# Performance work log

Hardware: AMD Instinct MI355X
Metric: run time of the kernel (lower is better)

The kernel has to match this reference:

```python
import jax, jax.numpy as jnp
from jax import lax
import numpy as np

N_BASIS = 256
N_FREQ = 128
N_TIME = 8
LAM = 0.2
LR = 1e-3
B1, B2, EPS = 0.9, 0.999, 1e-8
CONV_TOL = 1e-3


def setup_inputs() -> dict:
    key = jax.random.key(0)
    k1, k2 = jax.random.split(key)
    spec = jax.random.normal(k1, (32, N_FREQ, 256), dtype=jnp.float32)
    basis = jax.random.normal(k2, (N_FREQ * N_TIME, N_BASIS), dtype=jnp.float32)
    return {"spec": spec, "basis": basis, "n_iter_coef": 30, "pad": 0, "stride": 4}


def normalize01(x):
    # torch normalize01 with dims=-1, keepdims
    xmin = x.min(axis=-1, keepdims=True)
    xmax = x.max(axis=-1, keepdims=True)
    return (x - xmin) / (xmax - xmin)


def _response(x, basis, n_iter):
    # x: [B, D]; Adam-optimize coef [B, N_BASIS] for n_iter steps with the
    # same early-stop rule as the torch code (frozen via a done flag).
    B = x.shape[0]
    sig = jnp.std(x, ddof=1)  # torch .std() is unbiased over all elements

    def loss_fn(coef):
        pred = coef @ basis.T                      # [B, D]
        mse = jnp.mean((pred - x) ** 2)
        return mse + LAM * sig * jnp.mean(jnp.abs(coef / sig))

    coef0 = jnp.full((B, N_BASIS), 0.5 / N_BASIS, dtype=jnp.float32)
    m0 = jnp.zeros_like(coef0)
    v0 = jnp.zeros_like(coef0)

    def body(carry, _):
        coef, m, v, t, old_loss, done = carry
        loss, g = jax.value_and_grad(loss_fn)(coef)
        t_new = t + 1.0
        m_new = B1 * m + (1.0 - B1) * g
        v_new = B2 * v + (1.0 - B2) * g * g
        mhat = m_new / (1.0 - B1 ** t_new)
        vhat = v_new / (1.0 - B2 ** t_new)
        coef_new = coef - LR * mhat / (jnp.sqrt(vhat) + EPS)
        conv = jnp.abs(old_loss - loss) / old_loss < CONV_TOL
        sel = lambda a, b: jnp.where(done, a, b)
        new_carry = (
            sel(coef, coef_new),
            sel(m, m_new),
            sel(v, v_new),
            jnp.where(done, t, t_new),
            jnp.where(done, old_loss, loss),
            done | conv,
        )
        return new_carry, None

    init = (coef0, m0, v0, jnp.float32(0.0), jnp.float32(1e-10), jnp.array(False))
    (coef, _, _, _, _, _), _ = lax.scan(body, init, None, length=n_iter)
    return coef  # detached in torch


def reference(spec, basis, n_iter_coef, pad, stride):
    if spec.ndim == 2:
        spec = spec[None, ...]
    B, F, T = spec.shape
    spec_ = jnp.pad(spec, ((0, 0), (0, 0), (pad, pad)))
    starts = np.arange(0, T - N_TIME + 1, stride)          # window start frames
    idx = starts[:, None] + np.arange(N_TIME)              # [W, N_TIME]
    wins = spec_[:, :, idx]                                # [B, F, W, N_TIME]
    x = jnp.transpose(wins, (2, 0, 1, 3)).reshape(len(starts), B, F * N_TIME)
    x = normalize01(x)                                     # per row of [B, D]
    coef = jax.vmap(lambda xw: _response(xw, basis, n_iter_coef))(x)  # [W, B, N_BASIS]
    return jnp.transpose(coef, (1, 2, 0))                  # [B, N_BASIS, W]
```

## Files before the change

kernel.cpp:

```cpp
#include <hip/hip_runtime.h>
#include <math.h>

#define NB     256
#define NF     128
#define FT     1024
#define NW     63
#define TORIG  256
#define MAXIT  48
#define RPB    8
#define NBLK   4
#define GRID   256

__device__ __forceinline__ float rl(float v, int lane) {
    return __uint_as_float((unsigned)__builtin_amdgcn_readlane((int)__float_as_uint(v), lane));
}

__device__ __forceinline__ int xidx(int k2, int cg, int row) {
    return (k2 * 512 + row * 64 + (cg ^ row)) * 4;
}

__global__ __launch_bounds__(512, 2) void window_kernel(
    const float* __restrict__ spec,
    const float* __restrict__ basis,
    float* __restrict__ G,
    const int* __restrict__ p_niter,
    const int* __restrict__ p_pad,
    const int* __restrict__ p_stride,
    double* __restrict__ sxbuf,
    double* __restrict__ gpart,
    unsigned int* __restrict__ gcnt,
    float* __restrict__ out)
{
    __shared__ float  s_p0[RPB * 2048];
    __shared__ float  s_p1[RPB * 2048];
    __shared__ float  s_gred[2][NB];
    __shared__ float  s_mn[RPB], s_rng[RPB];
    __shared__ double s_dred[8];
    __shared__ float  s_redq[2][8], s_redr[2][8];
    __shared__ unsigned int s_wcnt[2];
    __shared__ int    s_stop[2];
    float* const s_xn = s_p1;

    const int bid = blockIdx.x;
    const int yy  = bid >> 3;
    const int q   = yy & 3;
    const int w   = (bid & 7) + 8 * (yy >> 2);
    const int tid = threadIdx.x;
    const int ks  = tid >> 6;
    const int kg  = tid & 63;
    const int r   = kg >> 3;
    const int cgo = 8 * ks + (kg & 7);
    const int n_iter = p_niter[0];
    const int t0     = w * p_stride[0] - p_pad[0];
    unsigned int* gbar = gcnt + MAXIT * NW;

    {
        const int c = tid & 255, jh = tid >> 8;
        float acc = 0.f;
        const float* bp = basis + (size_t)(jh * 512) * NB;
        #pragma unroll 16
        for (int j = 0; j < 512; ++j)
            acc = fmaf(bp[j * NB + bid], bp[j * NB + c], acc);
        s_gred[jh][c] = acc;
        __syncthreads();
        if (jh == 0) G[(size_t)bid * NB + c] = s_gred[0][c] + s_gred[1][c];
    }
    __threadfence();
    __syncthreads();
    if (tid == 0) atomicAdd(gbar, 1u);
    if (w >= NW) return;

    #pragma unroll
    for (int i = 0; i < 16; ++i) {
        const int e = i * 512 + tid;
        const int b = e >> 10, jj = e & 1023;
        const int f = jj >> 3, t = jj & 7, tq = t0 + t;
        s_xn[b * FT + jj] = (tq >= 0 && tq < TORIG)
            ? spec[((size_t)(q * RPB + b) * NF + f) * TORIG + tq] : 0.f;
    }
    __syncthreads();
    {
        float mn = __builtin_inff(), mx = -__builtin_inff();
        #pragma unroll
        for (int i = 0; i < 16; ++i) {
            const float v = s_xn[ks * FT + i * 64 + kg];
            mn = fminf(mn, v); mx = fmaxf(mx, v);
        }
        #pragma unroll
        for (int off = 32; off; off >>= 1) {
            mn = fminf(mn, __shfl_down(mn, off));
            mx = fmaxf(mx, __shfl_down(mx, off));
        }
        if (kg == 0) { s_mn[ks] = mn; s_rng[ks] = mx - mn; }
    }
    __syncthreads();
    double sx2p = 0.0;
    #pragma unroll
    for (int i = 0; i < 16; ++i) {
        const int e = i * 512 + tid;
        const int b = e >> 10, jj = e & 1023;
        const float v = (s_xn[b * FT + jj] - s_mn[b]) / s_rng[b];
        s_xn[b * FT + jj] = v;
        sx2p += (double)v * (double)v;
    }
    #pragma unroll
    for (int off = 32; off; off >>= 1) sx2p += __shfl_down(sx2p, off);
    if (kg == 0) s_dred[ks] = sx2p;
    __syncthreads();
    if (tid == 0) {
        double s = 0.0;
        #pragma unroll
        for (int i = 0; i < 8; ++i) s += s_dred[i];
        sxbuf[w * NBLK + q] = s;
        __threadfence();
    }

    float xbp[RPB][4];
    #pragma unroll
    for (int b = 0; b < RPB; ++b)
        #pragma unroll
        for (int j = 0; j < 4; ++j) xbp[b][j] = 0.f;
    for (int i0 = 0; i0 < 128; i0 += 4) {
        const int jj = ks * 128 + i0;
        float4 bv[4];
        #pragma unroll
        for (int t = 0; t < 4; ++t)
            bv[t] = *(const float4*)(basis + (size_t)(jj + t) * NB + 4 * kg);
        #pragma unroll
        for (int b = 0; b < RPB; ++b) {
            const float4 x4 = *(const float4*)&s_xn[b * FT + jj];
            xbp[b][0] = fmaf(x4.x, bv[0].x, fmaf(x4.y, bv[1].x, fmaf(x4.z, bv[2].x, fmaf(x4.w, bv[3].x, xbp[b][0]))));
            xbp[b][1] = fmaf(x4.x, bv[0].y, fmaf(x4.y, bv[1].y, fmaf(x4.z, bv[2].y, fmaf(x4.w, bv[3].y, xbp[b][1]))));
            xbp[b][2] = fmaf(x4.x, bv[0].z, fmaf(x4.y, bv[1].z, fmaf(x4.z, bv[2].z, fmaf(x4.w, bv[3].z, xbp[b][2]))));
            xbp[b][3] = fmaf(x4.x, bv[0].w, fmaf(x4.y, bv[1].w, fmaf(x4.z, bv[2].w, fmaf(x4.w, bv[3].w, xbp[b][3]))));
        }
    }
    __syncthreads();
    #pragma unroll
    for (int b = 0; b < RPB; ++b)
        *(float4*)&s_p0[xidx(ks, kg, b)] =
            make_float4(xbp[b][0], xbp[b][1], xbp[b][2], xbp[b][3]);
    __syncthreads();
    float xB[4] = {0.f, 0.f, 0.f, 0.f};
    #pragma unroll
    for (int k2 = 0; k2 < 8; ++k2) {
        const float4 p4 = *(const float4*)&s_p0[xidx(k2, cgo, r)];
        xB[0] += p4.x; xB[1] += p4.y; xB[2] += p4.z; xB[3] += p4.w;
    }

    if (tid == 0) {
        while (__hip_atomic_load(gbar, __ATOMIC_ACQUIRE, __HIP_MEMORY_SCOPE_AGENT) < (unsigned)GRID)
            __builtin_amdgcn_s_sleep(1);
    }
    if (tid == 64) { s_wcnt[0] = 0; s_wcnt[1] = 0; s_stop[0] = 0; s_stop[1] = 0; }
    __syncthreads();
    float4 g[32];
    #pragma unroll
    for (int kl = 0; kl < 32; ++kl)
        g[kl] = *(const float4*)(G + (size_t)(32 * ks + kl) * NB + 4 * kg);

    const float C0 = 0.5f / 256.f;
    float cf[4] = {C0, C0, C0, C0}, m_[4] = {0, 0, 0, 0}, v_[4] = {0, 0, 0, 0};
    float b1p = 1.f, b2p = 1.f;
    float old_loss = 1e-10f;
    double sxtot = 0.0;
    const float c1 = 2.f / 32768.f, c2 = 0.2f / 8192.f;

    for (int it = 0; it < n_iter; ++it) {
        const int p = it & 1;
        float* const sp = p ? s_p1 : s_p0;

        float pacc[RPB][4];
        #pragma unroll
        for (int b = 0; b < RPB; ++b)
            #pragma unroll
            for (int j = 0; j < 4; ++j) pacc[b][j] = 0.f;
        #pragma unroll
        for (int m = 0; m < 8; ++m) {
            const float4 ga = g[4 * m + 0], gb = g[4 * m + 1];
            const float4 gc = g[4 * m + 2], gd = g[4 * m + 3];
            #pragma unroll
            for (int b = 0; b < RPB; ++b) {
                const int L = b * 8 + m;
                const float cx = rl(cf[0], L), cy = rl(cf[1], L);
                const float cz = rl(cf[2], L), cw = rl(cf[3], L);
                pacc[b][0] = fmaf(cx, ga.x, fmaf(cy, gb.x, fmaf(cz, gc.x, fmaf(cw, gd.x, pacc[b][0]))));
                pacc[b][1] = fmaf(cx, ga.y, fmaf(cy, gb.y, fmaf(cz, gc.y, fmaf(cw, gd.y, pacc[b][1]))));
                pacc[b][2] = fmaf(cx, ga.z, fmaf(cy, gb.z, fmaf(cz, gc.z, fmaf(cw, gd.z, pacc[b][2]))));
                pacc[b][3] = fmaf(cx, ga.w, fmaf(cy, gb.w, fmaf(cz, gc.w, fmaf(cw, gd.w, pacc[b][3]))));
            }
        }
        #pragma unroll
        for (int b = 0; b < RPB; ++b)
            *(float4*)&sp[xidx(ks, kg, b)] =
                make_float4(pacc[b][0], pacc[b][1], pacc[b][2], pacc[b][3]);

        if (tid == 64 && it > 0) {
            while (__hip_atomic_load(&gcnt[(it - 1) * NW + w], __ATOMIC_ACQUIRE,
                                     __HIP_MEMORY_SCOPE_AGENT) < (unsigned)NBLK)
                __builtin_amdgcn_s_sleep(1);
            const size_t pbm = ((size_t)(it - 1) * NW + w) * NBLK;
            double Qt = 0.0, Rt = 0.0;
            #pragma unroll
            for (int i = 0; i < NBLK; ++i) {
                Qt += gpart[(pbm + i) * 2 + 0];
                Rt += gpart[(pbm + i) * 2 + 1];
            }
            if (it == 1)
                sxtot = sxbuf[w * NBLK + 0] + sxbuf[w * NBLK + 1] +
                        sxbuf[w * NBLK + 2] + sxbuf[w * NBLK + 3];
            const float loss = (float)((Qt + sxtot) / 32768.0 + 0.2 * (Rt / 8192.0));
            const float stat = fabsf(old_loss - loss) / old_loss;
            old_loss = loss;
            s_stop[p] = (stat < 1e-3f) ? 1 : 0;
        }

        __syncthreads();

        if (s_stop[p]) break;

        float a4[4] = {0.f, 0.f, 0.f, 0.f};
        #pragma unroll
        for (int k2 = 0; k2 < 8; ++k2) {
            const float4 p4 = *(const float4*)&sp[xidx(k2, cgo, r)];
            a4[0] += p4.x; a4[1] += p4.y; a4[2] += p4.z; a4[3] += p4.w;
        }

        float qc = 0.f, rr = 0.f;
        #pragma unroll
        for (int j = 0; j < 4; ++j) {
            qc += cf[j] * (a4[j] - 2.f * xB[j]);
            rr += fabsf(cf[j]);
        }
        #pragma unroll
        for (int off = 32; off; off >>= 1) {
            qc += __shfl_down(qc, off);
            rr += __shfl_down(rr, off);
        }
        if (kg == 0) {
            s_redq[p][ks] = qc; s_redr[p][ks] = rr;
            __threadfence_block();
            const unsigned old = __hip_atomic_fetch_add(&s_wcnt[p], 1u,
                                    __ATOMIC_ACQ_REL, __HIP_MEMORY_SCOPE_WORKGROUP);
            if (old == 7u) {
                float Q = 0.f, R = 0.f;
                #pragma unroll
                for (int i = 0; i < 8; ++i) { Q += s_redq[p][i]; R += s_redr[p][i]; }
                s_wcnt[p] = 0u;
                const size_t pb = ((size_t)it * NW + w) * NBLK;
                gpart[(pb + q) * 2 + 0] = (double)Q;
                gpart[(pb + q) * 2 + 1] = (double)R;
                __hip_atomic_fetch_add(&gcnt[it * NW + w], 1u,
                                       __ATOMIC_RELEASE, __HIP_MEMORY_SCOPE_AGENT);
            }
        }

        b1p *= 0.9f; b2p *= 0.999f;
        const float bc1 = 1.f - b1p, bc2 = 1.f - b2p;
        #pragma unroll
        for (int j = 0; j < 4; ++j) {
            const float c_ = cf[j];
            const float sgn = (c_ > 0.f) ? 1.f : ((c_ < 0.f) ? -1.f : 0.f);
            const float gg = c1 * (a4[j] - xB[j]) + c2 * sgn;
            m_[j] = 0.9f * m_[j] + 0.1f * gg;
            v_[j] = 0.999f * v_[j] + 0.001f * gg * gg;
            cf[j] = c_ - 1e-3f * (m_[j] / bc1) / (sqrtf(v_[j] / bc2) + 1e-8f);
        }
    }

    #pragma unroll
    for (int j = 0; j < 4; ++j)
        out[((size_t)(q * RPB + r) * NB + 4 * cgo + j) * NW + w] = cf[j];
}

extern "C" void kernel_launch(void* const* d_in, const int* in_sizes, int n_in,
                              void* d_out, int out_size, void* d_ws, size_t ws_size,
                              hipStream_t stream)
{
    const float* spec   = (const float*)d_in[0];
    const float* basis  = (const float*)d_in[1];
    const int* p_niter  = (const int*)d_in[2];
    const int* p_pad    = (const int*)d_in[3];
    const int* p_stride = (const int*)d_in[4];
    float* out = (float*)d_out;

    char* ws = (char*)d_ws;
    float*        G     = (float*)ws;
    double*       sxbuf = (double*)(ws + 262144);
    double*       gpart = (double*)(ws + 266240);
    unsigned int* gcnt  = (unsigned int*)(ws + 266240 + 193536);

    hipMemsetAsync(gcnt, 0, (MAXIT * NW + 1) * sizeof(unsigned int), stream);
    window_kernel<<<dim3(GRID), dim3(512), 0, stream>>>(
        spec, basis, G, p_niter, p_pad, p_stride, sxbuf, gpart, gcnt, out);
}
```

Measured before the change: 322.7 us.

## Delay the convergence check by one iteration to hide the cross-block loss wait

The early-stop loss check now waits for the global partial sums from two iterations back instead of one. This gives the cross-block atomic counter a full extra iteration to complete before the spin-wait. The coefficients from the previous step are kept so the output can roll back one step when the delayed check fires, and a post-loop check covers the final iteration. The matvec loop is also reordered per row to reduce live accumulators, and the bias-correction divides become reciprocal multiplies. The price is one speculative extra iteration of work before a stop, plus a tail synchronisation.

```diff
diff --git a/kernel.cpp b/kernel.cpp
--- a/kernel.cpp
+++ b/kernel.cpp
@@ -160,53 +160,31 @@
         g[kl] = *(const float4*)(G + (size_t)(32 * ks + kl) * NB + 4 * kg);
 
     const float C0 = 0.5f / 256.f;
-    float cf[4] = {C0, C0, C0, C0}, m_[4] = {0, 0, 0, 0}, v_[4] = {0, 0, 0, 0};
+    float cf[4]  = {C0, C0, C0, C0}, cfp[4] = {C0, C0, C0, C0};
+    float m_[4]  = {0, 0, 0, 0},    v_[4]  = {0, 0, 0, 0};
     float b1p = 1.f, b2p = 1.f;
     float old_loss = 1e-10f;
     double sxtot = 0.0;
     const float c1 = 2.f / 32768.f, c2 = 0.2f / 8192.f;
+    int use_prev = 0;
 
     for (int it = 0; it < n_iter; ++it) {
         const int p = it & 1;
         float* const sp = p ? s_p1 : s_p0;
 
-        float pacc[RPB][4];
-        #pragma unroll
-        for (int b = 0; b < RPB; ++b)
-            #pragma unroll
-            for (int j = 0; j < 4; ++j) pacc[b][j] = 0.f;
-        #pragma unroll
-        for (int m = 0; m < 8; ++m) {
-            const float4 ga = g[4 * m + 0], gb = g[4 * m + 1];
-            const float4 gc = g[4 * m + 2], gd = g[4 * m + 3];
-            #pragma unroll
-            for (int b = 0; b < RPB; ++b) {
-                const int L = b * 8 + m;
-                const float cx = rl(cf[0], L), cy = rl(cf[1], L);
-                const float cz = rl(cf[2], L), cw = rl(cf[3], L);
-                pacc[b][0] = fmaf(cx, ga.x, fmaf(cy, gb.x, fmaf(cz, gc.x, fmaf(cw, gd.x, pacc[b][0]))));
-                pacc[b][1] = fmaf(cx, ga.y, fmaf(cy, gb.y, fmaf(cz, gc.y, fmaf(cw, gd.y, pacc[b][1]))));
-                pacc[b][2] = fmaf(cx, ga.z, fmaf(cy, gb.z, fmaf(cz, gc.z, fmaf(cw, gd.z, pacc[b][2]))));
-                pacc[b][3] = fmaf(cx, ga.w, fmaf(cy, gb.w, fmaf(cz, gc.w, fmaf(cw, gd.w, pacc[b][3]))));
-            }
-        }
-        #pragma unroll
-        for (int b = 0; b < RPB; ++b)
-            *(float4*)&sp[xidx(ks, kg, b)] =
-                make_float4(pacc[b][0], pacc[b][1], pacc[b][2], pacc[b][3]);
-
-        if (tid == 64 && it > 0) {
-            while (__hip_atomic_load(&gcnt[(it - 1) * NW + w], __ATOMIC_ACQUIRE,
+        if (tid == 64 && it >= 2) {
+            const int itc = it - 2;
+            while (__hip_atomic_load(&gcnt[itc * NW + w], __ATOMIC_ACQUIRE,
                                      __HIP_MEMORY_SCOPE_AGENT) < (unsigned)NBLK)
                 __builtin_amdgcn_s_sleep(1);
-            const size_t pbm = ((size_t)(it - 1) * NW + w) * NBLK;
+            const size_t pbm = ((size_t)itc * NW + w) * NBLK;
             double Qt = 0.0, Rt = 0.0;
             #pragma unroll
             for (int i = 0; i < NBLK; ++i) {
                 Qt += gpart[(pbm + i) * 2 + 0];
                 Rt += gpart[(pbm + i) * 2 + 1];
             }
-            if (it == 1)
+            if (itc == 0)
                 sxtot = sxbuf[w * NBLK + 0] + sxbuf[w * NBLK + 1] +
                         sxbuf[w * NBLK + 2] + sxbuf[w * NBLK + 3];
             const float loss = (float)((Qt + sxtot) / 32768.0 + 0.2 * (Rt / 8192.0));
@@ -215,9 +193,27 @@
             s_stop[p] = (stat < 1e-3f) ? 1 : 0;
         }
 
+        #pragma unroll
+        for (int b = 0; b < RPB; ++b) {
+            float p0 = 0.f, p1 = 0.f, p2 = 0.f, p3 = 0.f;
+            #pragma unroll
+            for (int m = 0; m < 8; ++m) {
+                const float4 ga = g[4 * m + 0], gb = g[4 * m + 1];
+                const float4 gc = g[4 * m + 2], gd = g[4 * m + 3];
+                const int L = b * 8 + m;
+                const float cx = rl(cf[0], L), cy = rl(cf[1], L);
+                const float cz = rl(cf[2], L), cw = rl(cf[3], L);
+                p0 = fmaf(cx, ga.x, fmaf(cy, gb.x, fmaf(cz, gc.x, fmaf(cw, gd.x, p0))));
+                p1 = fmaf(cx, ga.y, fmaf(cy, gb.y, fmaf(cz, gc.y, fmaf(cw, gd.y, p1))));
+                p2 = fmaf(cx, ga.z, fmaf(cy, gb.z, fmaf(cz, gc.z, fmaf(cw, gd.z, p2))));
+                p3 = fmaf(cx, ga.w, fmaf(cy, gb.w, fmaf(cz, gc.w, fmaf(cw, gd.w, p3))));
+            }
+            *(float4*)&sp[xidx(ks, kg, b)] = make_float4(p0, p1, p2, p3);
+        }
+
         __syncthreads();
 
-        if (s_stop[p]) break;
+        if (s_stop[p]) { use_prev = 1; break; }
 
         float a4[4] = {0.f, 0.f, 0.f, 0.f};
         #pragma unroll
@@ -226,51 +222,79 @@
             a4[0] += p4.x; a4[1] += p4.y; a4[2] += p4.z; a4[3] += p4.w;
         }
 
-        float qc = 0.f, rr = 0.f;
-        #pragma unroll
-        for (int j = 0; j < 4; ++j) {
-            qc += cf[j] * (a4[j] - 2.f * xB[j]);
-            rr += fabsf(cf[j]);
-        }
-        #pragma unroll
-        for (int off = 32; off; off >>= 1) {
-            qc += __shfl_down(qc, off);
-            rr += __shfl_down(rr, off);
-        }
-        if (kg == 0) {
-            s_redq[p][ks] = qc; s_redr[p][ks] = rr;
-            __threadfence_block();
-            const unsigned old = __hip_atomic_fetch_add(&s_wcnt[p], 1u,
-                                    __ATOMIC_ACQ_REL, __HIP_MEMORY_SCOPE_WORKGROUP);
-            if (old == 7u) {
-                float Q = 0.f, R = 0.f;
-                #pragma unroll
-                for (int i = 0; i < 8; ++i) { Q += s_redq[p][i]; R += s_redr[p][i]; }
-                s_wcnt[p] = 0u;
-                const size_t pb = ((size_t)it * NW + w) * NBLK;
-                gpart[(pb + q) * 2 + 0] = (double)Q;
-                gpart[(pb + q) * 2 + 1] = (double)R;
-                __hip_atomic_fetch_add(&gcnt[it * NW + w], 1u,
-                                       __ATOMIC_RELEASE, __HIP_MEMORY_SCOPE_AGENT);
+        if (it + 1 < n_iter) {
+            float qc = 0.f, rr = 0.f;
+            #pragma unroll
+            for (int j = 0; j < 4; ++j) {
+                qc += cf[j] * (a4[j] - 2.f * xB[j]);
+                rr += fabsf(cf[j]);
+            }
+            #pragma unroll
+            for (int off = 32; off; off >>= 1) {
+                qc += __shfl_down(qc, off);
+                rr += __shfl_down(rr, off);
+            }
+            if (kg == 0) {
+                s_redq[p][ks] = qc; s_redr[p][ks] = rr;
+                __threadfence_block();
+                const unsigned old = __hip_atomic_fetch_add(&s_wcnt[p], 1u,
+                                        __ATOMIC_ACQ_REL, __HIP_MEMORY_SCOPE_WORKGROUP);
+                if (old == 7u) {
+                    float Q = 0.f, R = 0.f;
+                    #pragma unroll
+                    for (int i = 0; i < 8; ++i) { Q += s_redq[p][i]; R += s_redr[p][i]; }
+                    s_wcnt[p] = 0u;
+                    const size_t pb = ((size_t)it * NW + w) * NBLK;
+                    gpart[(pb + q) * 2 + 0] = (double)Q;
+                    gpart[(pb + q) * 2 + 1] = (double)R;
+                    __hip_atomic_fetch_add(&gcnt[it * NW + w], 1u,
+                                           __ATOMIC_RELEASE, __HIP_MEMORY_SCOPE_AGENT);
+                }
             }
         }
 
         b1p *= 0.9f; b2p *= 0.999f;
-        const float bc1 = 1.f - b1p, bc2 = 1.f - b2p;
+        const float rb1 = 1.f / (1.f - b1p), rb2 = 1.f / (1.f - b2p);
         #pragma unroll
         for (int j = 0; j < 4; ++j) {
             const float c_ = cf[j];
+            cfp[j] = c_;
             const float sgn = (c_ > 0.f) ? 1.f : ((c_ < 0.f) ? -1.f : 0.f);
             const float gg = c1 * (a4[j] - xB[j]) + c2 * sgn;
             m_[j] = 0.9f * m_[j] + 0.1f * gg;
             v_[j] = 0.999f * v_[j] + 0.001f * gg * gg;
-            cf[j] = c_ - 1e-3f * (m_[j] / bc1) / (sqrtf(v_[j] / bc2) + 1e-8f);
-        }
+            cf[j] = c_ - 1e-3f * (m_[j] * rb1) / (sqrtf(v_[j] * rb2) + 1e-8f);
+        }
+    }
+
+    if (!use_prev && n_iter >= 2) {
+        if (tid == 64) {
+            const int itc = n_iter - 2;
+            while (__hip_atomic_load(&gcnt[itc * NW + w], __ATOMIC_ACQUIRE,
+                                     __HIP_MEMORY_SCOPE_AGENT) < (unsigned)NBLK)
+                __builtin_amdgcn_s_sleep(1);
+            const size_t pbm = ((size_t)itc * NW + w) * NBLK;
+            double Qt = 0.0, Rt = 0.0;
+            #pragma unroll
+            for (int i = 0; i < NBLK; ++i) {
+                Qt += gpart[(pbm + i) * 2 + 0];
+                Rt += gpart[(pbm + i) * 2 + 1];
+            }
+            if (itc == 0)
+                sxtot = sxbuf[w * NBLK + 0] + sxbuf[w * NBLK + 1] +
+                        sxbuf[w * NBLK + 2] + sxbuf[w * NBLK + 3];
+            const float loss = (float)((Qt + sxtot) / 32768.0 + 0.2 * (Rt / 8192.0));
+            const float stat = fabsf(old_loss - loss) / old_loss;
+            s_stop[0] = (stat < 1e-3f) ? 1 : 0;
+        }
+        __syncthreads();
+        use_prev = s_stop[0];
     }
 
     #pragma unroll
     for (int j = 0; j < 4; ++j)
-        out[((size_t)(q * RPB + r) * NB + 4 * cgo + j) * NW + w] = cf[j];
+        out[((size_t)(q * RPB + r) * NB + 4 * cgo + j) * NW + w] =
+            use_prev ? cfp[j] : cf[j];
 }
 
 extern "C" void kernel_launch(void* const* d_in, const int* in_sizes, int n_in,
```

Measured after the change: 312.1 us. 3.3% less time.
